# Kernel optimization log

Hardware: AMD Instinct MI355X
Metric: run time of the kernel (lower is better)

The kernel has to match this reference:

```python
import jax, jax.numpy as jnp
import numpy as np

C_IN, D_STATE, EXPAND, KS = 64, 16, 2, 3
D_INNER = EXPAND * C_IN
HP_KS, HP_SIGMA = 15, 3.0
B, H, W = 4, 256, 256


def _gauss2d(ks, sigma):
    ax = jnp.arange(ks, dtype=jnp.float32) - (ks - 1) / 2.0
    g = jnp.exp(-(ax ** 2) / (2.0 * sigma ** 2))
    g = g / g.sum()
    return jnp.outer(g, g)


def _dwconv(x, w, pad):
    # x: [B,d,H,W], w: [d,1,kh,kw] depthwise
    return jax.lax.conv_general_dilated(
        x, w, window_strides=(1, 1), padding=[(pad, pad), (pad, pad)],
        dimension_numbers=("NCHW", "OIHW", "NCHW"),
        feature_group_count=x.shape[1])


def _selective_scan(u, dt, Bm, Cm, A, D, scan_axis):
    # u, dt: [B,d,H,W]; Bm, Cm: [B,N,H,W]; scan over scan_axis (2 or 3)
    u_s = jnp.moveaxis(u, scan_axis, 0)    # [L,B,d,M]
    dt_s = jnp.moveaxis(dt, scan_axis, 0)
    B_s = jnp.moveaxis(Bm, scan_axis, 0)   # [L,B,N,M]
    C_s = jnp.moveaxis(Cm, scan_axis, 0)
    Bb, d = u.shape[0], u.shape[1]
    M = u_s.shape[-1]
    N = A.shape[1]

    def step(h, inp):
        uj, dtj, Bj, Cj = inp                     # [B,d,M], [B,d,M], [B,N,M], [B,N,M]
        expA = jnp.exp(dtj[..., None] * A[None, :, None, :])   # [B,d,M,N]
        Bt = jnp.transpose(Bj, (0, 2, 1))[:, None]              # [B,1,M,N]
        Ct = jnp.transpose(Cj, (0, 2, 1))[:, None]
        h = expA * h + (uj * dtj)[..., None] * Bt               # [B,d,M,N]
        y = jnp.sum(h * Ct, axis=-1) + D[None, :, None] * uj    # [B,d,M]
        return h, y

    h0 = jnp.zeros((Bb, d, M, N), u.dtype)
    _, ys = jax.lax.scan(step, h0, (u_s, dt_s, B_s, C_s))
    return jnp.moveaxis(ys, 0, scan_axis)


def setup_inputs() -> dict:
    key = jax.random.key(0)
    ks = jax.random.split(key, 12)
    d, N = D_INNER, D_STATE
    A_log = -(jnp.linspace(0.0, 1.0, N, dtype=jnp.float32) * jnp.log(10.0))
    A_log = jnp.broadcast_to(A_log[None, :], (d, N)).astype(jnp.float32)
    return {
        "x": jax.random.normal(ks[0], (B, C_IN, H, W), jnp.float32),
        "in_proj_w": jax.random.normal(ks[1], (2 * d, C_IN), jnp.float32) * 0.05,
        "in_proj_b": jnp.zeros((2 * d,), jnp.float32),
        "dw_w": jax.random.normal(ks[2], (d, 1, KS, KS), jnp.float32) * 0.2,
        "dw_b": jnp.zeros((d,), jnp.float32),
        "xproj_w": jax.random.normal(ks[3], (1 + 2 * N, d), jnp.float32) * 0.05,
        "dtproj_w": jax.random.normal(ks[4], (d, 1), jnp.float32) * 0.5,
        "dtproj_b": jax.random.normal(ks[5], (d,), jnp.float32) * 0.5 - 4.0,
        "A_log": A_log,
        "D": jnp.ones((d,), jnp.float32),
        "out_w": jax.random.normal(ks[6], (C_IN, d), jnp.float32) * 0.05,
        "out_b": jnp.zeros((C_IN,), jnp.float32),
    }


def reference(x, in_proj_w, in_proj_b, dw_w, dw_b, xproj_w,
              dtproj_w, dtproj_b, A_log, D, out_w, out_b):
    d, N = D_INNER, D_STATE
    # in_proj (1x1 conv)
    uz = jnp.einsum("bchw,oc->bohw", x, in_proj_w) + in_proj_b[None, :, None, None]
    U, Z = uz[:, :d], uz[:, d:]
    # depthwise conv
    Uc = _dwconv(U, dw_w, KS // 2) + dw_b[None, :, None, None]
    # tanh(alpha * x) * weight + bias with alpha=0.5, weight=1, bias=0
    Uc = jnp.tanh(0.5 * Uc)
    # Gaussian high-pass: x - depthwise gaussian blur
    g = _gauss2d(HP_KS, HP_SIGMA)
    gk = jnp.broadcast_to(g[None, None], (d, 1, HP_KS, HP_KS))
    Uc = Uc - _dwconv(Uc, gk, HP_KS // 2)
    # x_proj (1x1 conv, no bias)
    params = jnp.einsum("bchw,oc->bohw", Uc, xproj_w)
    delta_in = params[:, :1]                 # [B,1,H,W]
    B_map = params[:, 1:1 + N]               # [B,N,H,W]
    C_map = params[:, 1 + N:1 + 2 * N]
    dt = jax.nn.softplus(jnp.einsum("bohw,do->bdhw", delta_in, dtproj_w)
                         + dtproj_b[None, :, None, None])
    A = -jnp.exp(A_log)
    Y_h = _selective_scan(Uc, dt, B_map, C_map, A, D, scan_axis=3)   # scan over W
    Y_v = _selective_scan(Y_h, dt, B_map, C_map, A, D, scan_axis=2)  # scan over H
    out = Y_v * jax.nn.sigmoid(Z)
    return jnp.einsum("bdhw,cd->bchw", out, out_w) + out_b[None, :, None, None]
```

## Files before the change

### kernel.cpp

```cpp
#include <hip/hip_runtime.h>
#include <hip/hip_bf16.h>
#include <math.h>

#define BB 4
#define CIN 64
#define DI 128
#define NS 16
#define HH 256
#define WW 256
#define HW 65536
#define NCH_P 33

__device__ __forceinline__ float softplusf(float x) {
    return fmaxf(x, 0.f) + __logf(1.0f + __expf(-fabsf(x)));
}
__device__ __forceinline__ float tanh_half(float a) {
    return 1.0f - 2.0f / (1.0f + __expf(a));
}
__device__ __forceinline__ float sigmoidf(float z) {
    return 1.0f / (1.0f + __expf(-z));
}

__device__ __forceinline__ void gauss15(float* g) {
    float s = 0.f;
#pragma unroll
    for (int i = 0; i < 15; ++i) {
        float a = (float)i - 7.0f;
        g[i] = __expf(-a * a / 18.0f);
        s += g[i];
    }
    float inv = 1.0f / s;
#pragma unroll
    for (int i = 0; i < 15; ++i) g[i] *= inv;
}

__global__ __launch_bounds__(256) void k_inproj(
    const float* __restrict__ xb, const float* __restrict__ w,
    const float* __restrict__ bias, float* __restrict__ Ub) {
    int p = blockIdx.x * 256 + threadIdx.x;
    int og = blockIdx.y * 64;
    float xv[CIN];
#pragma unroll
    for (int c = 0; c < CIN; ++c) xv[c] = xb[(size_t)c * HW + p];
#pragma unroll 2
    for (int o = og; o < og + 64; ++o) {
        float a0 = bias[o], a1 = 0.f, a2 = 0.f, a3 = 0.f;
        const float* wr = w + o * CIN;
#pragma unroll
        for (int c = 0; c < CIN; c += 4) {
            a0 = fmaf(xv[c],     wr[c],     a0);
            a1 = fmaf(xv[c + 1], wr[c + 1], a1);
            a2 = fmaf(xv[c + 2], wr[c + 2], a2);
            a3 = fmaf(xv[c + 3], wr[c + 3], a3);
        }
        Ub[(size_t)o * HW + p] = (a0 + a1) + (a2 + a3);
    }
}

#define TILE_H 16
__global__ __launch_bounds__(256) void k_conv(
    const float* __restrict__ Ub, const float* __restrict__ dww,
    const float* __restrict__ dwb, float* __restrict__ Ucb) {
    __shared__ float sU[32 * 256];
    __shared__ float sC[30 * 272];
    int c  = blockIdx.x >> 4;
    int t  = blockIdx.x & 15;
    int h0 = t * TILE_H;
    int w  = threadIdx.x;

    const float* base = Ub + (size_t)c * HW;
#pragma unroll
    for (int i = 0; i < 32; ++i) {
        int hh = h0 + i - 8;
        sU[i * 256 + w] = (hh >= 0 && hh < HH) ? base[hh * WW + w] : 0.f;
    }
    __syncthreads();

    float wt[9];
#pragma unroll
    for (int i = 0; i < 9; ++i) wt[i] = dww[c * 9 + i];
    float bb = dwb[c];

#pragma unroll
    for (int i = 0; i < 30; ++i) {
        int r = h0 + i - 7;
        float v = 0.f;
        if (r >= 0 && r < HH) {
            float acc = bb;
#pragma unroll
            for (int ky = 0; ky < 3; ++ky) {
                const float* ur = sU + (i + ky) * 256;
#pragma unroll
                for (int kx = 0; kx < 3; ++kx) {
                    int ww = w + kx - 1;
                    if (ww >= 0 && ww < WW) acc = fmaf(ur[ww], wt[ky * 3 + kx], acc);
                }
            }
            v = tanh_half(acc);
        }
        sC[i * 272 + w + 7] = v;
    }
    if (w < 7) {
#pragma unroll
        for (int i = 0; i < 30; ++i) { sC[i * 272 + w] = 0.f; sC[i * 272 + w + 263] = 0.f; }
    }
    __syncthreads();

    float g[15]; gauss15(g);
#pragma unroll
    for (int i = 0; i < 30; ++i) {
        float acc = 0.f;
#pragma unroll
        for (int k = 0; k < 15; ++k) acc = fmaf(sC[i * 272 + w + k], g[k], acc);
        sU[i * 256 + w] = acc;
    }
    float* outp = Ucb + (size_t)c * HW + h0 * WW + w;
#pragma unroll
    for (int i = 0; i < TILE_H; ++i) {
        float acc = 0.f;
#pragma unroll
        for (int k = 0; k < 15; ++k) acc = fmaf(sU[(i + k) * 256 + w], g[k], acc);
        float center = sC[(i + 7) * 272 + w + 7];
        outp[i * WW] = center - acc;
    }
}

__global__ __launch_bounds__(256) void k_xproj(
    const float* __restrict__ Uc, const float* __restrict__ xw,
    float* __restrict__ P) {
    int p = blockIdx.x * 256 + threadIdx.x;
    int b = p >> 16;
    int rem = p & 65535;
    const float* up = Uc + (size_t)b * DI * HW + rem;
    float acc[NCH_P];
#pragma unroll
    for (int o = 0; o < NCH_P; ++o) acc[o] = 0.f;
    for (int c = 0; c < DI; ++c) {
        float u = up[(size_t)c * HW];
#pragma unroll
        for (int o = 0; o < NCH_P; ++o) acc[o] = fmaf(u, xw[o * DI + c], acc[o]);
    }
    float* pp = P + (size_t)b * NCH_P * HW + rem;
#pragma unroll
    for (int o = 0; o < NCH_P; ++o) pp[(size_t)o * HW] = acc[o];
}

#define CW 32
__global__ __launch_bounds__(128) void k_scan_w(
    float* __restrict__ UY, const float* __restrict__ P,
    const float* __restrict__ A_log, const float* __restrict__ dtw,
    const float* __restrict__ dtb, const float* __restrict__ Dv) {
    __shared__ float sU[DI * 33];
    __shared__ float sP[CW * 36];
    int bh = blockIdx.x;
    int b = bh >> 8;
    int h = bh & 255;
    int t = threadIdx.x;

    float Av[NS];
#pragma unroll
    for (int n = 0; n < NS; ++n) Av[n] = -__expf(A_log[t * NS + n]);
    float wdt = dtw[t], bdt = dtb[t], Dd = Dv[t];
    float hS[NS];
#pragma unroll
    for (int n = 0; n < NS; ++n) hS[n] = 0.f;

    float* ubase = UY + (size_t)(b * DI) * HW + (size_t)h * WW;
    const float* prow = P + (size_t)(b * NCH_P) * HW + (size_t)h * WW;

    const int w4 = (t & 7) * 4;
    const int dbase = t >> 3;

    float4 rU[8];
    float rP[9];
#pragma unroll
    for (int p = 0; p < 8; ++p)
        rU[p] = *(const float4*)(ubase + (size_t)(dbase + p * 16) * HW + w4);
#pragma unroll
    for (int i = 0; i < 9; ++i) {
        int idx = i * 128 + t, ch = idx >> 5, wi = idx & 31;
        rP[i] = (ch < NCH_P) ? prow[(size_t)ch * HW + wi] : 0.f;
    }

    for (int w0 = 0; w0 < WW; w0 += CW) {
#pragma unroll
        for (int p = 0; p < 8; ++p) {
            float* s = sU + (dbase + p * 16) * 33 + w4;
            s[0] = rU[p].x; s[1] = rU[p].y; s[2] = rU[p].z; s[3] = rU[p].w;
        }
#pragma unroll
        for (int i = 0; i < 9; ++i) {
            int idx = i * 128 + t, ch = idx >> 5, wi = idx & 31;
            if (ch < NCH_P) sP[wi * 36 + ch] = rP[i];
        }
        __syncthreads();
        if (w0 + CW < WW) {
#pragma unroll
            for (int p = 0; p < 8; ++p)
                rU[p] = *(const float4*)(ubase + (size_t)(dbase + p * 16) * HW + w0 + CW + w4);
#pragma unroll
            for (int i = 0; i < 9; ++i) {
                int idx = i * 128 + t, ch = idx >> 5, wi = idx & 31;
                rP[i] = (ch < NCH_P) ? prow[(size_t)ch * HW + w0 + CW + wi] : 0.f;
            }
        }
#pragma unroll 2
        for (int wi = 0; wi < CW; ++wi) {
            const float* pr = sP + wi * 36;
            float4 q0 = *(const float4*)(pr);
            float4 q1 = *(const float4*)(pr + 4);
            float4 q2 = *(const float4*)(pr + 8);
            float4 q3 = *(const float4*)(pr + 12);
            float4 q4 = *(const float4*)(pr + 16);
            float4 q5 = *(const float4*)(pr + 20);
            float4 q6 = *(const float4*)(pr + 24);
            float4 q7 = *(const float4*)(pr + 28);
            float q8 = pr[32];
            float u = sU[t * 33 + wi];
            float dt = softplusf(fmaf(q0.x, wdt, bdt));
            float ud = u * dt;
            float y = Dd * u;
            float Bv[NS] = {q0.y,q0.z,q0.w,q1.x,q1.y,q1.z,q1.w,q2.x,
                            q2.y,q2.z,q2.w,q3.x,q3.y,q3.z,q3.w,q4.x};
            float Cv[NS] = {q4.y,q4.z,q4.w,q5.x,q5.y,q5.z,q5.w,q6.x,
                            q6.y,q6.z,q6.w,q7.x,q7.y,q7.z,q7.w,q8};
#pragma unroll
            for (int n = 0; n < NS; ++n) {
                float e = __expf(dt * Av[n]);
                hS[n] = fmaf(e, hS[n], ud * Bv[n]);
                y = fmaf(hS[n], Cv[n], y);
            }
            sU[t * 33 + wi] = y;
        }
        __syncthreads();
#pragma unroll
        for (int p = 0; p < 8; ++p) {
            const float* s = sU + (dbase + p * 16) * 33 + w4;
            float4 v; v.x = s[0]; v.y = s[1]; v.z = s[2]; v.w = s[3];
            *(float4*)(ubase + (size_t)(dbase + p * 16) * HW + w0 + w4) = v;
        }
        __syncthreads();
    }
}

#define WT2 64

#define LD2(hb) { \
    _Pragma("unroll") for (int rr = 0; rr < 2; ++rr) { \
        int hp = (hb) + rr; if (hp > HH - 1) hp = HH - 1; \
        const float* pr_ = pt + hp * WW; \
        _Pragma("unroll") for (int k = 0; k < 8; ++k) rp[rr][k] = pr_[(size_t)(4 * k) * HW]; \
        rp8[rr] = (dl == 0) ? pr_[(size_t)32 * HW] : 0.f; \
    } }
#define WR2(bf) { \
    _Pragma("unroll") for (int rr = 0; rr < 2; ++rr) { \
        _Pragma("unroll") for (int k = 0; k < 8; ++k) sP[bf][rr][4 * k + dl][wl] = rp[rr][k]; \
        if (dl == 0) sP[bf][rr][32][wl] = rp8[rr]; \
    } }
#define PU2(uu, hp_) { int hp = (hp_); if (hp > HH - 1) hp = HH - 1; uu = ub[hp * WW]; }
#define CP2(bf, rr, hh, uu) { \
    const float* pr_ = &sP[bf][rr][0][wl]; \
    float de = pr_[0]; \
    float dt = softplusf(fmaf(de, wdt, bdt)); \
    float ud = (uu) * dt; \
    float y = Dd * (uu); \
    _Pragma("unroll") for (int n = 0; n < NS; ++n) { \
        float e = __expf(dt * Av[n]); \
        hS[n] = fmaf(e, hS[n], ud * pr_[(1 + n) * WT2]); \
        y = fmaf(hS[n], pr_[(17 + n) * WT2], y); } \
    ub[(hh) * WW] = y; }

__global__ __launch_bounds__(256) void k_scan_h(
    float* __restrict__ UY, const float* __restrict__ P,
    const float* __restrict__ A_log, const float* __restrict__ dtw,
    const float* __restrict__ dtb, const float* __restrict__ Dv) {
    __shared__ float sP[2][2][NCH_P][WT2];
    int bid = blockIdx.x;
    int b  = bid >> 7;
    int r  = bid & 127;
    int wt = r >> 5;
    int dg = r & 31;
    int t  = threadIdx.x;
    int dl = t >> 6;
    int wl = t & 63;
    int d  = dg * 4 + dl;

    float Av[NS];
#pragma unroll
    for (int n = 0; n < NS; ++n) Av[n] = -__expf(A_log[d * NS + n]);
    float wdt = dtw[d], bdt = dtb[d], Dd = Dv[d];
    float hS[NS];
#pragma unroll
    for (int n = 0; n < NS; ++n) hS[n] = 0.f;

    float* ub = UY + (size_t)(b * DI + d) * HW + wt * WT2 + wl;
    const float* pt = P + (size_t)b * NCH_P * HW + (size_t)dl * HW + wt * WT2 + wl;

    float rp[2][8], rp8[2];
    float uA0, uA1, uB0, uB1;

    LD2(0);
    PU2(uA0, 0); PU2(uA1, 1); PU2(uB0, 2); PU2(uB1, 3);
    WR2(0);
    __syncthreads();
    LD2(2);

#pragma unroll 1
    for (int h0 = 0; h0 < HH; h0 += 4) {
        CP2(0, 0, h0,     uA0);
        CP2(0, 1, h0 + 1, uA1);
        WR2(1);
        __syncthreads();
        LD2(h0 + 4);
        PU2(uA0, h0 + 4); PU2(uA1, h0 + 5);
        CP2(1, 0, h0 + 2, uB0);
        CP2(1, 1, h0 + 3, uB1);
        WR2(0);
        __syncthreads();
        LD2(h0 + 6);
        PU2(uB0, h0 + 6); PU2(uB1, h0 + 7);
    }
}

__global__ __launch_bounds__(256) void k_gate(
    float* __restrict__ Y, const float* __restrict__ x,
    const float* __restrict__ wz, const float* __restrict__ bz) {
    int p = blockIdx.x * 256 + threadIdx.x;
    int b = p >> 16;
    int rem = p & 65535;
    const float* xp = x + (size_t)b * CIN * HW + rem;
    float xv[CIN];
#pragma unroll
    for (int c = 0; c < CIN; ++c) xv[c] = xp[(size_t)c * HW];
    float* yp = Y + (size_t)b * DI * HW + rem;
#pragma unroll 2
    for (int dd = 0; dd < DI; ++dd) {
        float z0 = 0.f, z1 = 0.f, z2 = 0.f, z3 = 0.f;
        const float* wr = wz + dd * CIN;
#pragma unroll
        for (int c = 0; c < CIN; c += 4) {
            z0 = fmaf(xv[c],     wr[c],     z0);
            z1 = fmaf(xv[c + 1], wr[c + 1], z1);
            z2 = fmaf(xv[c + 2], wr[c + 2], z2);
            z3 = fmaf(xv[c + 3], wr[c + 3], z3);
        }
        float z = bz[dd] + ((z0 + z1) + (z2 + z3));
        float yv = yp[(size_t)dd * HW];
        yp[(size_t)dd * HW] = yv * sigmoidf(z);
    }
}

__global__ __launch_bounds__(256) void k_out2(
    const float* __restrict__ G, const float* __restrict__ ow,
    const float* __restrict__ ob, float* __restrict__ outp) {
    int p = blockIdx.x * 256 + threadIdx.x;
    int b = p >> 16;
    int rem = p & 65535;
    const float* gp = G + (size_t)b * DI * HW + rem;
    float acc[CIN];
#pragma unroll
    for (int c = 0; c < CIN; ++c) acc[c] = 0.f;
    for (int dd = 0; dd < DI; ++dd) {
        float g = gp[(size_t)dd * HW];
#pragma unroll
        for (int c = 0; c < CIN; ++c) acc[c] = fmaf(g, ow[c * DI + dd], acc[c]);
    }
    float* op = outp + (size_t)b * CIN * HW + rem;
#pragma unroll
    for (int c = 0; c < CIN; ++c) op[(size_t)c * HW] = acc[c] + ob[c];
}

extern "C" void kernel_launch(void* const* d_in, const int* in_sizes, int n_in,
                              void* d_out, int out_size, void* d_ws, size_t ws_size,
                              hipStream_t stream) {
    const float* x     = (const float*)d_in[0];
    const float* ipw   = (const float*)d_in[1];
    const float* ipb   = (const float*)d_in[2];
    const float* dww   = (const float*)d_in[3];
    const float* dwb   = (const float*)d_in[4];
    const float* xpw   = (const float*)d_in[5];
    const float* dtw   = (const float*)d_in[6];
    const float* dtb   = (const float*)d_in[7];
    const float* A_log = (const float*)d_in[8];
    const float* Dv    = (const float*)d_in[9];
    const float* ow    = (const float*)d_in[10];
    const float* ob    = (const float*)d_in[11];
    float* out = (float*)d_out;

    const float* wz = ipw + (size_t)DI * CIN;
    const float* bz = ipb + DI;

    const size_t PLANE = (size_t)DI * HW;
    const size_t NB    = (size_t)BB * PLANE;

    if (ws_size >= (NB + PLANE) * sizeof(float)) {
        float* bufY = (float*)d_ws;
        float* bufU = bufY + NB;
        float* P    = out;
        for (int b = 0; b < BB; ++b) {
            k_inproj<<<dim3(HW / 256, 2), 256, 0, stream>>>(x + (size_t)b * CIN * HW, ipw, ipb, bufU);
            k_conv<<<DI * 16, 256, 0, stream>>>(bufU, dww, dwb, bufY + (size_t)b * PLANE);
        }
        k_xproj<<<BB * (HW / 256), 256, 0, stream>>>(bufY, xpw, P);
        k_scan_w<<<BB * HH, 128, 0, stream>>>(bufY, P, A_log, dtw, dtb, Dv);
        k_scan_h<<<BB * 128, 256, 0, stream>>>(bufY, P, A_log, dtw, dtb, Dv);
        k_gate<<<BB * (HW / 256), 256, 0, stream>>>(bufY, x, wz, bz);
        k_out2<<<BB * (HW / 256), 256, 0, stream>>>(bufY, ow, ob, out);
    } else {
        float* bufA = (float*)d_ws;
        float* bufY = bufA + PLANE;
        for (int b = 0; b < BB; ++b) {
            const float* xb = x + (size_t)b * CIN * HW;
            k_inproj<<<dim3(HW / 256, 2), 256, 0, stream>>>(xb, ipw, ipb, bufA);
            k_conv<<<DI * 16, 256, 0, stream>>>(bufA, dww, dwb, bufY);
            k_xproj<<<HW / 256, 256, 0, stream>>>(bufY, xpw, bufA);
            k_scan_w<<<HH, 128, 0, stream>>>(bufY, bufA, A_log, dtw, dtb, Dv);
            k_scan_h<<<128, 256, 0, stream>>>(bufY, bufA, A_log, dtw, dtb, Dv);
            k_gate<<<HW / 256, 256, 0, stream>>>(bufY, xb, wz, bz);
            k_out2<<<HW / 256, 256, 0, stream>>>(bufY, ow, ob, out + (size_t)b * CIN * HW);
        }
    }
}
```

Measured before the change: 1.463 ms.

## Precompute sigmoid gate in in-proj, fuse gate into tiled out-proj, deepen h-scan buffering

The in-projection kernel now also computes the Z half and stores sigmoid(Z) into a new workspace buffer. This lets a new shared-memory-tiled output projection multiply Y by the gate on the fly, removing the separate gate kernel and its extra read/write pass over Y. The vertical scan now stages four rows per buffer instead of two, halving the barriers per row. The trade-offs are a larger workspace requirement, an extra 128-channel Z buffer write and read, and more shared memory and registers in the scan.

```diff
diff --git a/kernel.cpp b/kernel.cpp
--- a/kernel.cpp
+++ b/kernel.cpp
@@ -34,26 +34,44 @@
     for (int i = 0; i < 15; ++i) g[i] *= inv;
 }
 
-__global__ __launch_bounds__(256) void k_inproj(
+__global__ __launch_bounds__(256) void k_inproj4(
     const float* __restrict__ xb, const float* __restrict__ w,
-    const float* __restrict__ bias, float* __restrict__ Ub) {
+    const float* __restrict__ bias, float* __restrict__ Ub,
+    float* __restrict__ Zb) {
     int p = blockIdx.x * 256 + threadIdx.x;
     int og = blockIdx.y * 64;
     float xv[CIN];
 #pragma unroll
     for (int c = 0; c < CIN; ++c) xv[c] = xb[(size_t)c * HW + p];
+    if (og < DI) {
 #pragma unroll 2
-    for (int o = og; o < og + 64; ++o) {
-        float a0 = bias[o], a1 = 0.f, a2 = 0.f, a3 = 0.f;
-        const float* wr = w + o * CIN;
-#pragma unroll
-        for (int c = 0; c < CIN; c += 4) {
-            a0 = fmaf(xv[c],     wr[c],     a0);
-            a1 = fmaf(xv[c + 1], wr[c + 1], a1);
-            a2 = fmaf(xv[c + 2], wr[c + 2], a2);
-            a3 = fmaf(xv[c + 3], wr[c + 3], a3);
-        }
-        Ub[(size_t)o * HW + p] = (a0 + a1) + (a2 + a3);
+        for (int o = og; o < og + 64; ++o) {
+            float a0 = bias[o], a1 = 0.f, a2 = 0.f, a3 = 0.f;
+            const float* wr = w + o * CIN;
+#pragma unroll
+            for (int c = 0; c < CIN; c += 4) {
+                a0 = fmaf(xv[c],     wr[c],     a0);
+                a1 = fmaf(xv[c + 1], wr[c + 1], a1);
+                a2 = fmaf(xv[c + 2], wr[c + 2], a2);
+                a3 = fmaf(xv[c + 3], wr[c + 3], a3);
+            }
+            Ub[(size_t)o * HW + p] = (a0 + a1) + (a2 + a3);
+        }
+    } else {
+#pragma unroll 2
+        for (int o = og; o < og + 64; ++o) {
+            float z0 = 0.f, z1 = 0.f, z2 = 0.f, z3 = 0.f;
+            const float* wr = w + o * CIN;
+#pragma unroll
+            for (int c = 0; c < CIN; c += 4) {
+                z0 = fmaf(xv[c],     wr[c],     z0);
+                z1 = fmaf(xv[c + 1], wr[c + 1], z1);
+                z2 = fmaf(xv[c + 2], wr[c + 2], z2);
+                z3 = fmaf(xv[c + 3], wr[c + 3], z3);
+            }
+            float z = bias[o] + ((z0 + z1) + (z2 + z3));
+            Zb[(size_t)(o - DI) * HW + p] = sigmoidf(z);
+        }
     }
 }
 
@@ -245,20 +263,20 @@
 
 #define WT2 64
 
-#define LD2(hb) { \
-    _Pragma("unroll") for (int rr = 0; rr < 2; ++rr) { \
+#define LD4(hb) { \
+    _Pragma("unroll") for (int rr = 0; rr < 4; ++rr) { \
         int hp = (hb) + rr; if (hp > HH - 1) hp = HH - 1; \
         const float* pr_ = pt + hp * WW; \
         _Pragma("unroll") for (int k = 0; k < 8; ++k) rp[rr][k] = pr_[(size_t)(4 * k) * HW]; \
         rp8[rr] = (dl == 0) ? pr_[(size_t)32 * HW] : 0.f; \
     } }
-#define WR2(bf) { \
-    _Pragma("unroll") for (int rr = 0; rr < 2; ++rr) { \
+#define WR4(bf) { \
+    _Pragma("unroll") for (int rr = 0; rr < 4; ++rr) { \
         _Pragma("unroll") for (int k = 0; k < 8; ++k) sP[bf][rr][4 * k + dl][wl] = rp[rr][k]; \
         if (dl == 0) sP[bf][rr][32][wl] = rp8[rr]; \
     } }
-#define PU2(uu, hp_) { int hp = (hp_); if (hp > HH - 1) hp = HH - 1; uu = ub[hp * WW]; }
-#define CP2(bf, rr, hh, uu) { \
+#define PU4(uu, hp_) { int hp = (hp_); if (hp > HH - 1) hp = HH - 1; uu = ub[hp * WW]; }
+#define CP4(bf, rr, hh, uu) { \
     const float* pr_ = &sP[bf][rr][0][wl]; \
     float de = pr_[0]; \
     float dt = softplusf(fmaf(de, wdt, bdt)); \
@@ -274,7 +292,7 @@
     float* __restrict__ UY, const float* __restrict__ P,
     const float* __restrict__ A_log, const float* __restrict__ dtw,
     const float* __restrict__ dtb, const float* __restrict__ Dv) {
-    __shared__ float sP[2][2][NCH_P][WT2];
+    __shared__ float sP[2][4][NCH_P][WT2];
     int bid = blockIdx.x;
     int b  = bid >> 7;
     int r  = bid & 127;
@@ -296,29 +314,36 @@
     float* ub = UY + (size_t)(b * DI + d) * HW + wt * WT2 + wl;
     const float* pt = P + (size_t)b * NCH_P * HW + (size_t)dl * HW + wt * WT2 + wl;
 
-    float rp[2][8], rp8[2];
-    float uA0, uA1, uB0, uB1;
-
-    LD2(0);
-    PU2(uA0, 0); PU2(uA1, 1); PU2(uB0, 2); PU2(uB1, 3);
-    WR2(0);
+    float rp[4][8], rp8[4];
+    float u0, u1, u2, u3, u4, u5, u6, u7;
+
+    LD4(0);
+    PU4(u0, 0); PU4(u1, 1); PU4(u2, 2); PU4(u3, 3);
+    PU4(u4, 4); PU4(u5, 5); PU4(u6, 6); PU4(u7, 7);
+    WR4(0);
     __syncthreads();
-    LD2(2);
+    LD4(4);
 
 #pragma unroll 1
-    for (int h0 = 0; h0 < HH; h0 += 4) {
-        CP2(0, 0, h0,     uA0);
-        CP2(0, 1, h0 + 1, uA1);
-        WR2(1);
-        __syncthreads();
-        LD2(h0 + 4);
-        PU2(uA0, h0 + 4); PU2(uA1, h0 + 5);
-        CP2(1, 0, h0 + 2, uB0);
-        CP2(1, 1, h0 + 3, uB1);
-        WR2(0);
-        __syncthreads();
-        LD2(h0 + 6);
-        PU2(uB0, h0 + 6); PU2(uB1, h0 + 7);
+    for (int h0 = 0; h0 < HH; h0 += 8) {
+        CP4(0, 0, h0,     u0);
+        CP4(0, 1, h0 + 1, u1);
+        CP4(0, 2, h0 + 2, u2);
+        CP4(0, 3, h0 + 3, u3);
+        WR4(1);
+        __syncthreads();
+        LD4(h0 + 8);
+        PU4(u0, h0 + 8);  PU4(u1, h0 + 9);
+        PU4(u2, h0 + 10); PU4(u3, h0 + 11);
+        CP4(1, 0, h0 + 4, u4);
+        CP4(1, 1, h0 + 5, u5);
+        CP4(1, 2, h0 + 6, u6);
+        CP4(1, 3, h0 + 7, u7);
+        WR4(0);
+        __syncthreads();
+        LD4(h0 + 12);
+        PU4(u4, h0 + 12); PU4(u5, h0 + 13);
+        PU4(u6, h0 + 14); PU4(u7, h0 + 15);
     }
 }
 
@@ -368,6 +393,69 @@
     float* op = outp + (size_t)b * CIN * HW + rem;
 #pragma unroll
     for (int c = 0; c < CIN; ++c) op[(size_t)c * HW] = acc[c] + ob[c];
+}
+
+__global__ __launch_bounds__(256) void k_out2g(
+    const float* __restrict__ Y, const float* __restrict__ Z,
+    const float* __restrict__ ow, const float* __restrict__ ob,
+    float* __restrict__ outp) {
+    __shared__ float sOw[64 * 129];
+    __shared__ float sG[32 * 64];
+    int t = threadIdx.x;
+    int bid = blockIdx.x;
+    int b   = bid >> 10;
+    int pxb = (bid & 1023) << 6;
+
+#pragma unroll
+    for (int i = 0; i < 32; ++i) {
+        int idx = i * 256 + t;
+        int c = idx >> 7, k = idx & 127;
+        sOw[c * 129 + k] = ow[c * DI + k];
+    }
+
+    const int c0  = (t >> 4) * 4;
+    const int px0 = (t & 15) * 4;
+    const int ks  = t >> 3;
+    const int pq  = (t & 7) * 8;
+
+    float4 acc[4];
+#pragma unroll
+    for (int i = 0; i < 4; ++i) acc[i] = make_float4(0.f, 0.f, 0.f, 0.f);
+
+    for (int kk0 = 0; kk0 < DI; kk0 += 32) {
+        __syncthreads();
+        const float* yr = Y + (size_t)(b * DI + kk0 + ks) * HW + pxb + pq;
+        const float* zr = Z + (size_t)(b * DI + kk0 + ks) * HW + pxb + pq;
+        float4 ya = *(const float4*)(yr);
+        float4 yb = *(const float4*)(yr + 4);
+        float4 za = *(const float4*)(zr);
+        float4 zb = *(const float4*)(zr + 4);
+        float4 ga, gb;
+        ga.x = ya.x * za.x; ga.y = ya.y * za.y; ga.z = ya.z * za.z; ga.w = ya.w * za.w;
+        gb.x = yb.x * zb.x; gb.y = yb.y * zb.y; gb.z = yb.z * zb.z; gb.w = yb.w * zb.w;
+        *(float4*)&sG[ks * 64 + pq]     = ga;
+        *(float4*)&sG[ks * 64 + pq + 4] = gb;
+        __syncthreads();
+#pragma unroll
+        for (int k = 0; k < 32; ++k) {
+            float4 g = *(const float4*)&sG[k * 64 + px0];
+#pragma unroll
+            for (int ci = 0; ci < 4; ++ci) {
+                float wv = sOw[(c0 + ci) * 129 + kk0 + k];
+                acc[ci].x = fmaf(g.x, wv, acc[ci].x);
+                acc[ci].y = fmaf(g.y, wv, acc[ci].y);
+                acc[ci].z = fmaf(g.z, wv, acc[ci].z);
+                acc[ci].w = fmaf(g.w, wv, acc[ci].w);
+            }
+        }
+    }
+#pragma unroll
+    for (int ci = 0; ci < 4; ++ci) {
+        float o = ob[c0 + ci];
+        float4 r = acc[ci];
+        r.x += o; r.y += o; r.z += o; r.w += o;
+        *(float4*)(outp + (size_t)(b * CIN + c0 + ci) * HW + pxb + px0) = r;
+    }
 }
 
 extern "C" void kernel_launch(void* const* d_in, const int* in_sizes, int n_in,
@@ -393,12 +481,27 @@
     const size_t PLANE = (size_t)DI * HW;
     const size_t NB    = (size_t)BB * PLANE;
 
-    if (ws_size >= (NB + PLANE) * sizeof(float)) {
+    if (ws_size >= (2 * NB + PLANE) * sizeof(float)) {
+        float* bufY = (float*)d_ws;
+        float* bufZ = bufY + NB;
+        float* bufU = bufZ + NB;
+        float* P    = out;
+        for (int b = 0; b < BB; ++b) {
+            k_inproj4<<<dim3(HW / 256, 4), 256, 0, stream>>>(
+                x + (size_t)b * CIN * HW, ipw, ipb, bufU, bufZ + (size_t)b * PLANE);
+            k_conv<<<DI * 16, 256, 0, stream>>>(bufU, dww, dwb, bufY + (size_t)b * PLANE);
+        }
+        k_xproj<<<BB * (HW / 256), 256, 0, stream>>>(bufY, xpw, P);
+        k_scan_w<<<BB * HH, 128, 0, stream>>>(bufY, P, A_log, dtw, dtb, Dv);
+        k_scan_h<<<BB * 128, 256, 0, stream>>>(bufY, P, A_log, dtw, dtb, Dv);
+        k_out2g<<<BB * 1024, 256, 0, stream>>>(bufY, bufZ, ow, ob, out);
+    } else if (ws_size >= (NB + PLANE) * sizeof(float)) {
         float* bufY = (float*)d_ws;
         float* bufU = bufY + NB;
         float* P    = out;
         for (int b = 0; b < BB; ++b) {
-            k_inproj<<<dim3(HW / 256, 2), 256, 0, stream>>>(x + (size_t)b * CIN * HW, ipw, ipb, bufU);
+            k_inproj4<<<dim3(HW / 256, 2), 256, 0, stream>>>(
+                x + (size_t)b * CIN * HW, ipw, ipb, bufU, bufU);
             k_conv<<<DI * 16, 256, 0, stream>>>(bufU, dww, dwb, bufY + (size_t)b * PLANE);
         }
         k_xproj<<<BB * (HW / 256), 256, 0, stream>>>(bufY, xpw, P);
@@ -411,7 +514,7 @@
         float* bufY = bufA + PLANE;
         for (int b = 0; b < BB; ++b) {
             const float* xb = x + (size_t)b * CIN * HW;
-            k_inproj<<<dim3(HW / 256, 2), 256, 0, stream>>>(xb, ipw, ipb, bufA);
+            k_inproj4<<<dim3(HW / 256, 2), 256, 0, stream>>>(xb, ipw, ipb, bufA, bufA);
             k_conv<<<DI * 16, 256, 0, stream>>>(bufA, dww, dwb, bufY);
             k_xproj<<<HW / 256, 256, 0, stream>>>(bufY, xpw, bufA);
             k_scan_w<<<HH, 128, 0, stream>>>(bufY, bufA, A_log, dtw, dtb, Dv);
```

New measurement: 1.471 ms. No clear change (+0.5%).
